# Kernel tuning notes

Hardware: AMD Instinct MI355X
Metric: run time of the kernel (lower is better)

Reference implementation:

```python
import jax, jax.numpy as jnp
import numpy as np

B, T, C, HS = 8, 2048, 1024, 128


def setup_inputs() -> dict:
    key = jax.random.key(0)
    k1, k2, k3, k4 = jax.random.split(key, 4)
    return {
        "x": jax.random.normal(k1, (B, T, C), dtype=jnp.float32),
        "Wq": jax.random.normal(k2, (C, HS), dtype=jnp.float32) * (C ** -0.5),
        "Wk": jax.random.normal(k3, (C, HS), dtype=jnp.float32) * (C ** -0.5),
        "Wv": jax.random.normal(k4, (C, HS), dtype=jnp.float32) * (C ** -0.5),
    }


def _rope_tables(T, hs):
    # Matches get_rotary_embedding: d = hs//2, theta_i = 10000**(-2*(i-1)/d) for i in 0..d-1
    d = hs // 2
    i = jnp.arange(d, dtype=jnp.float32)
    theta = 10000.0 ** (-2.0 * (i - 1.0) / d)
    ang = jnp.arange(T, dtype=jnp.float32)[:, None] * theta[None, :]  # [T, d]
    return jnp.cos(ang), jnp.sin(ang)


def _rotate(t, c, s):
    # t: [B,T,hs]. Equivalent to t_m @ R_m with block-diag 2x2 rotations [[c,-s],[s,c]]:
    # out[2i] = e*c + o*s ; out[2i+1] = -e*s + o*c
    e, o = t[..., 0::2], t[..., 1::2]
    return jnp.stack([e * c + o * s, -e * s + o * c], axis=-1).reshape(t.shape)


def reference(x, Wq, Wk, Wv):
    Bx, Tx, Cx = x.shape
    hs = Wq.shape[1]
    c, s = _rope_tables(Tx, hs)
    q = _rotate(x @ Wq, c, s)  # [B,T,hs]
    k = _rotate(x @ Wk, c, s)
    v = x @ Wv
    scores = jnp.einsum("bqh,bkh->bqk", q, k) * (hs ** -0.5)  # [B,T,T]
    mask = jnp.tril(jnp.ones((Tx, Tx), dtype=bool))
    scores = jnp.where(mask, scores, -jnp.inf)
    A = jax.nn.softmax(scores, axis=-1)
    return jnp.einsum("bqk,bkh->bqh", A, v)
```

## Files before the change

kernel.cpp:

```cpp
#include <hip/hip_runtime.h>

typedef __bf16 bf16x8 __attribute__((ext_vector_type(8)));
typedef float f32x4 __attribute__((ext_vector_type(4)));

typedef const unsigned int __attribute__((address_space(1)))* gptr_t;
typedef unsigned int __attribute__((address_space(3)))* lptr_t;

static __device__ __forceinline__ unsigned short f2bf(float f){
  __bf16 h = (__bf16)f;
  return __builtin_bit_cast(unsigned short, h);
}
static __device__ __forceinline__ float bf2f(unsigned short h){
  unsigned int u = ((unsigned int)h) << 16;
  return __builtin_bit_cast(float, u);
}

__global__ __launch_bounds__(256) void k_prepw(const float* __restrict__ Wq,
                                               const float* __restrict__ Wk,
                                               const float* __restrict__ Wv,
                                               unsigned short* __restrict__ Wtb){
  int idx = blockIdx.x * 256 + threadIdx.x;
  int m = idx >> 10;
  int k = idx & 1023;
  const float* W = (m < 128) ? Wq : ((m < 256) ? Wk : Wv);
  int n = m & 127;
  Wtb[idx] = f2bf(W[k * 128 + n]);
}

__global__ __launch_bounds__(512) void k_qkv(const float* __restrict__ x,
                                             const unsigned short* __restrict__ Wtb,
                                             unsigned short* __restrict__ Qr,
                                             unsigned short* __restrict__ Kr,
                                             unsigned short* __restrict__ Vt){
  __shared__ __align__(16) unsigned short lds[64 * 64 + 128 * 64];

  unsigned short* sA = lds;
  unsigned short* sB = lds + 64 * 64;

  int bid0 = blockIdx.x;
  int wg = (bid0 & 7) * 96 + (bid0 >> 3);
  int mblk = wg / 3;
  int nblk = wg - mblk * 3;

  int tid = threadIdx.x;
  int lane = tid & 63, wid = tid >> 6;
  int wm = wid >> 1, wn = wid & 1;
  int g = lane >> 4, lr = lane & 15;

  f32x4 acc[4] = {};
  const float* xbase = x + (size_t)(mblk * 64) * 1024;
  const unsigned short* wbase = Wtb + (size_t)(nblk * 128) * 1024;

  int ar = tid >> 3, ac = tid & 7;
  const float* agp = xbase + (size_t)ar * 1024 + ac * 8;
  char* awp = (char*)sA + ar * 128 + (((ac ^ (ar & 7))) << 4);
  int bp = tid & 7;
  int br1 = tid >> 3, br2 = br1 + 64;
  const unsigned short* bgp1 = wbase + (size_t)br1 * 1024 + ((bp ^ (br1 & 7)) << 3);
  const unsigned short* bgp2 = wbase + (size_t)br2 * 1024 + ((bp ^ (br2 & 7)) << 3);
  unsigned short* bdst1 = sB + wid * 512;
  unsigned short* bdst2 = sB + 4096 + wid * 512;

  for (int t = 0; t < 16; t++){
    int k0 = t * 64;
    if (t) __syncthreads();
    __builtin_amdgcn_global_load_lds((gptr_t)(const void*)(bgp1 + k0),
                                     (lptr_t)(void*)bdst1, 16, 0, 0);
    __builtin_amdgcn_global_load_lds((gptr_t)(const void*)(bgp2 + k0),
                                     (lptr_t)(void*)bdst2, 16, 0, 0);
    float4 v0 = *reinterpret_cast<const float4*>(agp + k0);
    float4 v1 = *reinterpret_cast<const float4*>(agp + k0 + 4);
    union { bf16x8 h; uint4 u4; } pk;
    pk.h[0] = (__bf16)v0.x; pk.h[1] = (__bf16)v0.y;
    pk.h[2] = (__bf16)v0.z; pk.h[3] = (__bf16)v0.w;
    pk.h[4] = (__bf16)v1.x; pk.h[5] = (__bf16)v1.y;
    pk.h[6] = (__bf16)v1.z; pk.h[7] = (__bf16)v1.w;
    *reinterpret_cast<uint4*>(awp) = pk.u4;
    __syncthreads();

    int arow = wm * 16 + lr;
    int asw = (arow & 7) << 4;
#pragma unroll
    for (int ks = 0; ks < 2; ks++){
      bf16x8 af = *reinterpret_cast<const bf16x8*>(
          (const char*)sA + arow * 128 + ((ks * 64 + g * 16) ^ asw));
#pragma unroll
      for (int n = 0; n < 4; n++){
        int brow = wn * 64 + n * 16 + lr;
        bf16x8 bn = *reinterpret_cast<const bf16x8*>(
            (const char*)sB + brow * 128 + ((ks * 64 + g * 16) ^ ((brow & 7) << 4)));
        acc[n] = __builtin_amdgcn_mfma_f32_16x16x32_bf16(af, bn, acc[n], 0, 0, 0);
      }
    }
  }
  __syncthreads();

  int row0 = mblk * 64;
  if (nblk < 2){
    unsigned short* sE = lds;
    float scale = nblk ? 1.0f : 0.12751744950370064f;
#pragma unroll
    for (int n = 0; n < 4; n++){
      int col = wn * 64 + n * 16 + lr;
      int i = col >> 1;
      float theta = exp2f(13.287712379549449f * (2.0f - 2.0f * (float)i) * 0.015625f);
      float sgn = (lr & 1) ? -1.0f : 1.0f;
#pragma unroll
      for (int r = 0; r < 4; r++){
        int tl = wm * 16 + g * 4 + r;
        int t = (row0 + tl) & 2047;
        float s, c;
        sincosf((float)t * theta, &s, &c);
        float v = acc[n][r];
        float partner = __shfl_xor(v, 1);
        float res = (v * c + partner * sgn * s) * scale;
        sE[tl * 136 + col] = f2bf(res);
      }
    }
    __syncthreads();
    unsigned short* dst = (nblk ? Kr : Qr) + (size_t)row0 * 128;
#pragma unroll
    for (int p = 0; p < 2; p++){
      int u = tid + p * 512;
      int tl = u >> 4, h0 = (u & 15) * 8;
      uint4 vv = *reinterpret_cast<const uint4*>(&sE[tl * 136 + h0]);
      *reinterpret_cast<uint4*>(dst + (size_t)tl * 128 + h0) = vv;
    }
  } else {
    unsigned short* sE = lds;
#pragma unroll
    for (int n = 0; n < 4; n++){
      int col = wn * 64 + n * 16 + lr;
#pragma unroll
      for (int r = 0; r < 4; r++){
        int tl = wm * 16 + g * 4 + r;
        sE[col * 72 + tl] = f2bf(acc[n][r]);
      }
    }
    __syncthreads();
    int b = row0 >> 11;
    int t0 = row0 & 2047;
#pragma unroll
    for (int p = 0; p < 2; p++){
      int u = tid + p * 512;
      int h = u >> 3, tc = (u & 7) * 8;
      uint4 vv = *reinterpret_cast<const uint4*>(&sE[h * 72 + tc]);
      *reinterpret_cast<uint4*>(Vt + ((size_t)(b * 128 + h)) * 2048 + t0 + tc) = vv;
    }
  }
}

__global__ __launch_bounds__(128) void k_attn_part(const unsigned short* __restrict__ Qr,
                                                   const unsigned short* __restrict__ Kr,
                                                   const unsigned short* __restrict__ Vt,
                                                   unsigned short* __restrict__ Opart,
                                                   float* __restrict__ ml){
  __shared__ __align__(16) unsigned short sK[32][136];
  __shared__ __align__(16) unsigned short sV[128][40];
  __shared__ __align__(16) unsigned short sP[2][16][40];

  int bid = blockIdx.x;
  int b = bid / 160;
  int rem = bid - b * 160;
  int qt, c;
  if (rem < 16)      { qt = rem;                    c = 0; }
  else if (rem < 48) { qt = 16 + ((rem - 16) >> 1); c = (rem - 16) & 1; }
  else if (rem < 96) { int r2 = rem - 48; int d = r2 / 3; qt = 32 + d; c = r2 - 3 * d; }
  else               { int r3 = rem - 96; qt = 48 + (r3 >> 2); c = r3 & 3; }

  int q_base = qt * 32;
  int kv_start = c * 512;
  int kv_end = min(kv_start + 512, q_base + 32);
  int niter = (kv_end - kv_start) >> 5;

  int tid = threadIdx.x, w = tid >> 6, lane = tid & 63;
  int g = lane >> 4, lr = lane & 15;

  int qrow = q_base + w * 16 + lr;
  const unsigned short* qptr = Qr + ((size_t)(b * 2048 + qrow)) * 128;
  bf16x8 qf[4];
#pragma unroll
  for (int hc = 0; hc < 4; hc++)
    qf[hc] = *reinterpret_cast<const bf16x8*>(qptr + hc * 32 + g * 8);

  f32x4 oacc[8] = {};
  float mrow = -1e30f, lrow = 0.0f;

  const unsigned short* Kb = Kr + (size_t)b * 2048 * 128;
  const unsigned short* Vb = Vt + (size_t)b * 128 * 2048;

  for (int it = 0; it < niter; it++){
    int kv0 = kv_start + it * 32;
    __syncthreads();
#pragma unroll
    for (int p = 0; p < 4; p++){
      int idx = tid + p * 128;
      int r = idx >> 4, c8 = (idx & 15) * 8;
      *reinterpret_cast<uint4*>(&sK[r][c8]) =
        *reinterpret_cast<const uint4*>(Kb + (size_t)(kv0 + r) * 128 + c8);
    }
#pragma unroll
    for (int p = 0; p < 4; p++){
      int idx = tid + p * 128;
      int h = idx >> 2, c8 = (idx & 3) * 8;
      *reinterpret_cast<uint4*>(&sV[h][c8]) =
        *reinterpret_cast<const uint4*>(Vb + (size_t)h * 2048 + kv0 + c8);
    }
    __syncthreads();

    f32x4 st[2];
#pragma unroll
    for (int ct = 0; ct < 2; ct++){
      f32x4 a = {0.f, 0.f, 0.f, 0.f};
#pragma unroll
      for (int hc = 0; hc < 4; hc++){
        bf16x8 kf = *reinterpret_cast<const bf16x8*>(&sK[ct * 16 + lr][hc * 32 + g * 8]);
        a = __builtin_amdgcn_mfma_f32_16x16x32_bf16(kf, qf[hc], a, 0, 0, 0);
      }
      st[ct] = a;
    }

    float mx = -1e30f;
#pragma unroll
    for (int ct = 0; ct < 2; ct++){
      int kvb = kv0 + ct * 16 + g * 4;
#pragma unroll
      for (int r = 0; r < 4; r++){
        float s = (kvb + r <= qrow) ? st[ct][r] : -1e30f;
        st[ct][r] = s;
        mx = fmaxf(mx, s);
      }
    }
    mx = fmaxf(mx, __shfl_xor(mx, 16));
    mx = fmaxf(mx, __shfl_xor(mx, 32));
    float m = fmaxf(mrow, mx);
    float alpha = exp2f(mrow - m);

    float rs = 0.0f;
#pragma unroll
    for (int ct = 0; ct < 2; ct++){
      float p0 = exp2f(st[ct][0] - m);
      float p1 = exp2f(st[ct][1] - m);
      float p2 = exp2f(st[ct][2] - m);
      float p3 = exp2f(st[ct][3] - m);
      rs += (p0 + p1) + (p2 + p3);
      uint2 pk;
      pk.x = ((unsigned int)f2bf(p1) << 16) | f2bf(p0);
      pk.y = ((unsigned int)f2bf(p3) << 16) | f2bf(p2);
      *reinterpret_cast<uint2*>(&sP[w][lr][ct * 16 + g * 4]) = pk;
    }
    rs += __shfl_xor(rs, 16);
    rs += __shfl_xor(rs, 32);
    lrow = lrow * alpha + rs;
    mrow = m;

    float af0 = __shfl(alpha, g * 4 + 0);
    float af1 = __shfl(alpha, g * 4 + 1);
    float af2 = __shfl(alpha, g * 4 + 2);
    float af3 = __shfl(alpha, g * 4 + 3);
#pragma unroll
    for (int ht = 0; ht < 8; ht++){
      oacc[ht][0] *= af0;
      oacc[ht][1] *= af1;
      oacc[ht][2] *= af2;
      oacc[ht][3] *= af3;
    }

    bf16x8 pa = *reinterpret_cast<const bf16x8*>(&sP[w][lr][g * 8]);
#pragma unroll
    for (int ht = 0; ht < 8; ht++){
      bf16x8 vf = *reinterpret_cast<const bf16x8*>(&sV[ht * 16 + lr][g * 8]);
      oacc[ht] = __builtin_amdgcn_mfma_f32_16x16x32_bf16(pa, vf, oacc[ht], 0, 0, 0);
    }
  }

  size_t slot = (size_t)(b * 64 + qt) * 4 + c;
  unsigned short* op = Opart + slot * 4096;
  float* mlp = ml + slot * 64;
#pragma unroll
  for (int ht = 0; ht < 8; ht++)
#pragma unroll
    for (int r = 0; r < 4; r++){
      int rowl = w * 16 + g * 4 + r;
      op[rowl * 128 + ht * 16 + lr] = f2bf(oacc[ht][r]);
    }
  if (lane < 16){
    mlp[w * 16 + lr]      = mrow;
    mlp[32 + w * 16 + lr] = lrow;
  }
}

__global__ __launch_bounds__(256) void k_comb(const unsigned short* __restrict__ Opart,
                                              const float* __restrict__ ml,
                                              float* __restrict__ out){
  int bid = blockIdx.x;
  int b = bid >> 6, qt = bid & 63;
  int nck = (qt >> 4) + 1;
  int tid = threadIdx.x;
  int row = tid >> 3;
  int col0 = (tid & 7) * 16;
  size_t slot0 = (size_t)(b * 64 + qt) * 4;

  float m_c[4], l_c[4];
  float M = -1e30f;
#pragma unroll
  for (int c = 0; c < 4; c++) if (c < nck){
    m_c[c] = ml[(slot0 + c) * 64 + row];
    l_c[c] = ml[(slot0 + c) * 64 + 32 + row];
    M = fmaxf(M, m_c[c]);
  }
  float L = 0.0f, wgt[4];
#pragma unroll
  for (int c = 0; c < 4; c++) if (c < nck){
    wgt[c] = exp2f(m_c[c] - M);
    L += wgt[c] * l_c[c];
  }
  float acc[16] = {};
#pragma unroll
  for (int c = 0; c < 4; c++) if (c < nck){
    const unsigned short* src = Opart + (slot0 + c) * 4096 + row * 128 + col0;
    uint4 u0 = *reinterpret_cast<const uint4*>(src);
    uint4 u1 = *reinterpret_cast<const uint4*>(src + 8);
    unsigned int uu[8] = {u0.x, u0.y, u0.z, u0.w, u1.x, u1.y, u1.z, u1.w};
#pragma unroll
    for (int j = 0; j < 8; j++){
      acc[2 * j]     += wgt[c] * bf2f((unsigned short)(uu[j] & 0xFFFF));
      acc[2 * j + 1] += wgt[c] * bf2f((unsigned short)(uu[j] >> 16));
    }
  }
  float invL = 1.0f / L;
  float* dst = out + ((size_t)(b * 2048 + qt * 32 + row)) * 128 + col0;
#pragma unroll
  for (int j = 0; j < 4; j++){
    float4 v = {acc[4 * j] * invL, acc[4 * j + 1] * invL,
                acc[4 * j + 2] * invL, acc[4 * j + 3] * invL};
    *reinterpret_cast<float4*>(dst + 4 * j) = v;
  }
}

extern "C" void kernel_launch(void* const* d_in, const int* in_sizes, int n_in,
                              void* d_out, int out_size, void* d_ws, size_t ws_size,
                              hipStream_t stream) {
  const float* x  = (const float*)d_in[0];
  const float* Wq = (const float*)d_in[1];
  const float* Wk = (const float*)d_in[2];
  const float* Wv = (const float*)d_in[3];
  float* out = (float*)d_out;

  char* ws = (char*)d_ws;
  unsigned short* Wtb   = (unsigned short*)ws;
  unsigned short* Qr    = (unsigned short*)(ws + 786432);
  unsigned short* Kr    = (unsigned short*)(ws + 786432 + 4194304);
  unsigned short* Vt    = (unsigned short*)(ws + 786432 + 2*4194304);
  unsigned short* Opart = (unsigned short*)(ws + 786432 + 3*4194304);
  float* ml             = (float*)(ws + 786432 + 3*4194304 + 16777216);

  hipLaunchKernelGGL(k_prepw, dim3(1536), dim3(256), 0, stream, Wq, Wk, Wv, Wtb);
  hipLaunchKernelGGL(k_qkv,   dim3(768),  dim3(512), 0, stream, x, Wtb, Qr, Kr, Vt);
  hipLaunchKernelGGL(k_attn_part, dim3(1280), dim3(128), 0, stream, Qr, Kr, Vt, Opart, ml);
  hipLaunchKernelGGL(k_comb, dim3(512), dim3(256), 0, stream, Opart, ml, out);
}
```

Baseline: 77.39 us.

## Double-buffer LDS tiles in QKV projection GEMM to overlap loads with MFMA

Splits the QKV projection kernel's shared memory into two buffers. The next k-tile of weights (async global-to-LDS) and of x (held in registers, converted to bf16 after the MFMAs) is fetched while the current tile is being multiplied. This hides global load latency and drops one barrier per iteration. LDS use doubles, which can lower occupancy, and more registers stay live across the MFMA block.

```diff
diff --git a/kernel.cpp b/kernel.cpp
--- a/kernel.cpp
+++ b/kernel.cpp
@@ -27,15 +27,13 @@
   Wtb[idx] = f2bf(W[k * 128 + n]);
 }
 
+#define QKV_BUFS 12288
 __global__ __launch_bounds__(512) void k_qkv(const float* __restrict__ x,
                                              const unsigned short* __restrict__ Wtb,
                                              unsigned short* __restrict__ Qr,
                                              unsigned short* __restrict__ Kr,
                                              unsigned short* __restrict__ Vt){
-  __shared__ __align__(16) unsigned short lds[64 * 64 + 128 * 64];
-
-  unsigned short* sA = lds;
-  unsigned short* sB = lds + 64 * 64;
+  __shared__ __align__(16) unsigned short lds[2 * QKV_BUFS];
 
   int bid0 = blockIdx.x;
   int wg = (bid0 & 7) * 96 + (bid0 >> 3);
@@ -53,47 +51,75 @@
 
   int ar = tid >> 3, ac = tid & 7;
   const float* agp = xbase + (size_t)ar * 1024 + ac * 8;
-  char* awp = (char*)sA + ar * 128 + (((ac ^ (ar & 7))) << 4);
+  int awoff = ar * 128 + ((ac ^ (ar & 7)) << 4);
   int bp = tid & 7;
   int br1 = tid >> 3, br2 = br1 + 64;
   const unsigned short* bgp1 = wbase + (size_t)br1 * 1024 + ((bp ^ (br1 & 7)) << 3);
   const unsigned short* bgp2 = wbase + (size_t)br2 * 1024 + ((bp ^ (br2 & 7)) << 3);
-  unsigned short* bdst1 = sB + wid * 512;
-  unsigned short* bdst2 = sB + 4096 + wid * 512;
-
-  for (int t = 0; t < 16; t++){
-    int k0 = t * 64;
-    if (t) __syncthreads();
-    __builtin_amdgcn_global_load_lds((gptr_t)(const void*)(bgp1 + k0),
-                                     (lptr_t)(void*)bdst1, 16, 0, 0);
-    __builtin_amdgcn_global_load_lds((gptr_t)(const void*)(bgp2 + k0),
-                                     (lptr_t)(void*)bdst2, 16, 0, 0);
-    float4 v0 = *reinterpret_cast<const float4*>(agp + k0);
-    float4 v1 = *reinterpret_cast<const float4*>(agp + k0 + 4);
+  int bdoff1 = wid * 512;
+  int bdoff2 = 4096 + wid * 512;
+
+  {
+    unsigned short* sB = lds + 4096;
+    __builtin_amdgcn_global_load_lds((gptr_t)(const void*)bgp1,
+                                     (lptr_t)(void*)(sB + bdoff1), 16, 0, 0);
+    __builtin_amdgcn_global_load_lds((gptr_t)(const void*)bgp2,
+                                     (lptr_t)(void*)(sB + bdoff2), 16, 0, 0);
+    float4 v0 = *reinterpret_cast<const float4*>(agp);
+    float4 v1 = *reinterpret_cast<const float4*>(agp + 4);
     union { bf16x8 h; uint4 u4; } pk;
     pk.h[0] = (__bf16)v0.x; pk.h[1] = (__bf16)v0.y;
     pk.h[2] = (__bf16)v0.z; pk.h[3] = (__bf16)v0.w;
     pk.h[4] = (__bf16)v1.x; pk.h[5] = (__bf16)v1.y;
     pk.h[6] = (__bf16)v1.z; pk.h[7] = (__bf16)v1.w;
-    *reinterpret_cast<uint4*>(awp) = pk.u4;
-    __syncthreads();
-
-    int arow = wm * 16 + lr;
-    int asw = (arow & 7) << 4;
-#pragma unroll
-    for (int ks = 0; ks < 2; ks++){
-      bf16x8 af = *reinterpret_cast<const bf16x8*>(
-          (const char*)sA + arow * 128 + ((ks * 64 + g * 16) ^ asw));
-#pragma unroll
-      for (int n = 0; n < 4; n++){
-        int brow = wn * 64 + n * 16 + lr;
-        bf16x8 bn = *reinterpret_cast<const bf16x8*>(
-            (const char*)sB + brow * 128 + ((ks * 64 + g * 16) ^ ((brow & 7) << 4)));
-        acc[n] = __builtin_amdgcn_mfma_f32_16x16x32_bf16(af, bn, acc[n], 0, 0, 0);
-      }
-    }
-  }
-  __syncthreads();
+    *reinterpret_cast<uint4*>((char*)lds + awoff) = pk.u4;
+    __syncthreads();
+  }
+
+  int cur = 0;
+  float4 fa0, fa1;
+  for (int t = 0; t < 16; t++){
+    if (t < 15){
+      int k0n = (t + 1) * 64;
+      unsigned short* sB = lds + (cur ^ 1) * QKV_BUFS + 4096;
+      __builtin_amdgcn_global_load_lds((gptr_t)(const void*)(bgp1 + k0n),
+                                       (lptr_t)(void*)(sB + bdoff1), 16, 0, 0);
+      __builtin_amdgcn_global_load_lds((gptr_t)(const void*)(bgp2 + k0n),
+                                       (lptr_t)(void*)(sB + bdoff2), 16, 0, 0);
+      fa0 = *reinterpret_cast<const float4*>(agp + k0n);
+      fa1 = *reinterpret_cast<const float4*>(agp + k0n + 4);
+    }
+
+    {
+      const char* cA = (const char*)(lds + cur * QKV_BUFS);
+      const char* cB = cA + 8192;
+      int arow = wm * 16 + lr;
+      int asw = (arow & 7) << 4;
+#pragma unroll
+      for (int ks = 0; ks < 2; ks++){
+        bf16x8 af = *reinterpret_cast<const bf16x8*>(
+            cA + arow * 128 + ((ks * 64 + g * 16) ^ asw));
+#pragma unroll
+        for (int n = 0; n < 4; n++){
+          int brow = wn * 64 + n * 16 + lr;
+          bf16x8 bn = *reinterpret_cast<const bf16x8*>(
+              cB + brow * 128 + ((ks * 64 + g * 16) ^ ((brow & 7) << 4)));
+          acc[n] = __builtin_amdgcn_mfma_f32_16x16x32_bf16(af, bn, acc[n], 0, 0, 0);
+        }
+      }
+    }
+
+    if (t < 15){
+      union { bf16x8 h; uint4 u4; } pk;
+      pk.h[0] = (__bf16)fa0.x; pk.h[1] = (__bf16)fa0.y;
+      pk.h[2] = (__bf16)fa0.z; pk.h[3] = (__bf16)fa0.w;
+      pk.h[4] = (__bf16)fa1.x; pk.h[5] = (__bf16)fa1.y;
+      pk.h[6] = (__bf16)fa1.z; pk.h[7] = (__bf16)fa1.w;
+      *reinterpret_cast<uint4*>((char*)(lds + (cur ^ 1) * QKV_BUFS) + awoff) = pk.u4;
+    }
+    __syncthreads();
+    cur ^= 1;
+  }
 
   int row0 = mblk * 64;
   if (nblk < 2){
```

Measured after the change: 76.28 us. No clear change (-1.4%).

## Triple-buffer QKV projection loads with K-step 32 and raise MFMA priority in attention

Applied to the files above, without the earlier changes.

The QKV projection GEMM moves from a single-buffered 64-wide K loop with two barriers per step to a three-slot LDS ring with K-step 32. Global loads for step t+2 are issued while step t computes, and each step ends with one barrier after a waitcnt. The attention kernel also wraps its MFMA sections in s_setprio to favour matrix issue across waves. This aims to hide global-load latency in the projection, at the cost of more loop iterations, finer-grained waitcnt handling, and more LDS.

```diff
diff --git a/kernel.cpp b/kernel.cpp
--- a/kernel.cpp
+++ b/kernel.cpp
@@ -27,15 +27,13 @@
   Wtb[idx] = f2bf(W[k * 128 + n]);
 }
 
+#define QKV_BUF3 6144
 __global__ __launch_bounds__(512) void k_qkv(const float* __restrict__ x,
                                              const unsigned short* __restrict__ Wtb,
                                              unsigned short* __restrict__ Qr,
                                              unsigned short* __restrict__ Kr,
                                              unsigned short* __restrict__ Vt){
-  __shared__ __align__(16) unsigned short lds[64 * 64 + 128 * 64];
-
-  unsigned short* sA = lds;
-  unsigned short* sB = lds + 64 * 64;
+  __shared__ __align__(16) unsigned short lds[3 * QKV_BUF3];
 
   int bid0 = blockIdx.x;
   int wg = (bid0 & 7) * 96 + (bid0 >> 3);
@@ -52,46 +50,70 @@
   const unsigned short* wbase = Wtb + (size_t)(nblk * 128) * 1024;
 
   int ar = tid >> 3, ac = tid & 7;
-  const float* agp = xbase + (size_t)ar * 1024 + ac * 8;
-  char* awp = (char*)sA + ar * 128 + (((ac ^ (ar & 7))) << 4);
-  int bp = tid & 7;
-  int br1 = tid >> 3, br2 = br1 + 64;
-  const unsigned short* bgp1 = wbase + (size_t)br1 * 1024 + ((bp ^ (br1 & 7)) << 3);
-  const unsigned short* bgp2 = wbase + (size_t)br2 * 1024 + ((bp ^ (br2 & 7)) << 3);
-  unsigned short* bdst1 = sB + wid * 512;
-  unsigned short* bdst2 = sB + 4096 + wid * 512;
-
-  for (int t = 0; t < 16; t++){
-    int k0 = t * 64;
-    if (t) __syncthreads();
-    __builtin_amdgcn_global_load_lds((gptr_t)(const void*)(bgp1 + k0),
-                                     (lptr_t)(void*)bdst1, 16, 0, 0);
-    __builtin_amdgcn_global_load_lds((gptr_t)(const void*)(bgp2 + k0),
-                                     (lptr_t)(void*)bdst2, 16, 0, 0);
-    float4 v0 = *reinterpret_cast<const float4*>(agp + k0);
-    float4 v1 = *reinterpret_cast<const float4*>(agp + k0 + 4);
-    union { bf16x8 h; uint4 u4; } pk;
-    pk.h[0] = (__bf16)v0.x; pk.h[1] = (__bf16)v0.y;
-    pk.h[2] = (__bf16)v0.z; pk.h[3] = (__bf16)v0.w;
-    pk.h[4] = (__bf16)v1.x; pk.h[5] = (__bf16)v1.y;
-    pk.h[6] = (__bf16)v1.z; pk.h[7] = (__bf16)v1.w;
-    *reinterpret_cast<uint4*>(awp) = pk.u4;
-    __syncthreads();
-
-    int arow = wm * 16 + lr;
-    int asw = (arow & 7) << 4;
-#pragma unroll
-    for (int ks = 0; ks < 2; ks++){
+  const float* agp = xbase + (size_t)ar * 1024 + ac * 4;
+  int awoff = ar * 64 + (((ac >> 1) ^ (ar & 3)) << 4) + (ac & 1) * 8;
+  int br = tid >> 2, bc = tid & 3;
+  const unsigned short* bgp = wbase + (size_t)br * 1024 + ((bc ^ (br & 3)) << 3);
+  int bdoff = 2048 + wid * 512;
+
+  float4 faA;
+  {
+    float4 a0 = *reinterpret_cast<const float4*>(agp);
+    __builtin_amdgcn_global_load_lds((gptr_t)(const void*)bgp,
+                                     (lptr_t)(void*)(lds + bdoff), 16, 0, 0);
+    faA = *reinterpret_cast<const float4*>(agp + 32);
+    __builtin_amdgcn_global_load_lds((gptr_t)(const void*)(bgp + 32),
+                                     (lptr_t)(void*)(lds + QKV_BUF3 + bdoff), 16, 0, 0);
+    union { unsigned short s[4]; uint2 u2; } pk;
+    pk.s[0] = f2bf(a0.x); pk.s[1] = f2bf(a0.y);
+    pk.s[2] = f2bf(a0.z); pk.s[3] = f2bf(a0.w);
+    *reinterpret_cast<uint2*>((char*)lds + awoff) = pk.u2;
+    asm volatile("s_waitcnt vmcnt(2) lgkmcnt(0)" ::: "memory");
+    __builtin_amdgcn_s_barrier();
+    __builtin_amdgcn_sched_barrier(0);
+  }
+
+  for (int t = 0; t < 32; t++){
+    unsigned short* bufC = lds + (t % 3) * QKV_BUF3;
+    unsigned short* bufN = lds + ((t + 1) % 3) * QKV_BUF3;
+    unsigned short* bufF = lds + ((t + 2) % 3) * QKV_BUF3;
+    float4 fnA = faA;
+    if (t < 30){
+      int k0n = (t + 2) * 32;
+      fnA = *reinterpret_cast<const float4*>(agp + k0n);
+      __builtin_amdgcn_global_load_lds((gptr_t)(const void*)(bgp + k0n),
+                                       (lptr_t)(void*)(bufF + bdoff), 16, 0, 0);
+    }
+
+    {
+      const char* cA = (const char*)bufC;
+      const char* cB = cA + 4096;
+      int arow = wm * 16 + lr;
       bf16x8 af = *reinterpret_cast<const bf16x8*>(
-          (const char*)sA + arow * 128 + ((ks * 64 + g * 16) ^ asw));
+          cA + arow * 64 + ((g * 16) ^ ((arow & 3) << 4)));
 #pragma unroll
       for (int n = 0; n < 4; n++){
         int brow = wn * 64 + n * 16 + lr;
         bf16x8 bn = *reinterpret_cast<const bf16x8*>(
-            (const char*)sB + brow * 128 + ((ks * 64 + g * 16) ^ ((brow & 7) << 4)));
+            cB + brow * 64 + ((g * 16) ^ ((brow & 3) << 4)));
         acc[n] = __builtin_amdgcn_mfma_f32_16x16x32_bf16(af, bn, acc[n], 0, 0, 0);
       }
     }
+
+    if (t < 31){
+      union { unsigned short s[4]; uint2 u2; } pk;
+      pk.s[0] = f2bf(faA.x); pk.s[1] = f2bf(faA.y);
+      pk.s[2] = f2bf(faA.z); pk.s[3] = f2bf(faA.w);
+      *reinterpret_cast<uint2*>((char*)bufN + awoff) = pk.u2;
+
+      if (t < 30)
+        asm volatile("s_waitcnt vmcnt(2) lgkmcnt(0)" ::: "memory");
+      else
+        asm volatile("s_waitcnt vmcnt(0) lgkmcnt(0)" ::: "memory");
+      __builtin_amdgcn_s_barrier();
+      __builtin_amdgcn_sched_barrier(0);
+    }
+    faA = fnA;
   }
   __syncthreads();
 
@@ -209,6 +231,7 @@
     __syncthreads();
 
     f32x4 st[2];
+    __builtin_amdgcn_s_setprio(1);
 #pragma unroll
     for (int ct = 0; ct < 2; ct++){
       f32x4 a = {0.f, 0.f, 0.f, 0.f};
@@ -219,6 +242,7 @@
       }
       st[ct] = a;
     }
+    __builtin_amdgcn_s_setprio(0);
 
     float mx = -1e30f;
 #pragma unroll
@@ -267,11 +291,13 @@
     }
 
     bf16x8 pa = *reinterpret_cast<const bf16x8*>(&sP[w][lr][g * 8]);
+    __builtin_amdgcn_s_setprio(1);
 #pragma unroll
     for (int ht = 0; ht < 8; ht++){
       bf16x8 vf = *reinterpret_cast<const bf16x8*>(&sV[ht * 16 + lr][g * 8]);
       oacc[ht] = __builtin_amdgcn_mfma_f32_16x16x32_bf16(pa, vf, oacc[ht], 0, 0, 0);
     }
+    __builtin_amdgcn_s_setprio(0);
   }
 
   size_t slot = (size_t)(b * 64 + qt) * 4 + c;
```

Result: no change. 78.36 us (+1.3%).
